# Performance work log

Measured on AMD Instinct MI355X. Metric: run time of the kernel, lower is better.

Reference implementation:

```python
import jax, jax.numpy as jnp
import numpy as np

# PSLoss constants (from init_kwargs)
MSE_WEIGHT = 0.5
W_CORR = 1.0
W_VAR = 1.0
W_MEAN = 1.0
K = 3           # k_dominant_freqs
MIN_PATCH = 5   # min_patch_len (max(2, 5))
EPS = 1e-8


def setup_inputs() -> dict:
    key = jax.random.key(0)
    k1, k2 = jax.random.split(key)
    B, T, F = 64, 336, 321
    forecast = jax.random.normal(k1, (B, T, F), dtype=jnp.float32)
    target = jax.random.normal(k2, (B, T, F), dtype=jnp.float32)
    return {"forecast": forecast, "target": target}


def _structural_loss(fc, tg):
    """fc, tg: [N, T] flattened (batch*features) series. Returns (total_loss_sum, patch_count)."""
    N, T = tg.shape
    Mmax = T // MIN_PATCH  # max segments per period (period >= MIN_PATCH)

    # --- Fourier adaptive patching (vectorized over all N series) ---
    amp = jnp.abs(jnp.fft.rfft(tg, axis=-1))[:, 1:]           # drop DC, [N, T//2]
    _, rel = jax.lax.top_k(amp, K)                             # [N, K]
    freq_idx = (rel + 1).astype(jnp.float32)
    p = jnp.floor(T / freq_idx).astype(jnp.int32)              # dominant periods [N, K]
    # dedup periods in topk order (the original 'processed_periods' set)
    eq = p[:, :, None] == p[:, None, :]                        # [N, K, K]
    earlier = jnp.tril(jnp.ones((K, K), dtype=bool), -1)       # j < k
    dup = jnp.any(eq & earlier, axis=-1)
    valid_p = (p >= MIN_PATCH) & ~dup                          # [N, K]

    nseg = T // p                                              # [N, K] (p >= 2 always)
    s_idx = jnp.arange(Mmax, dtype=jnp.int32)
    seg_s = p[:, :, None] * s_idx                              # [N, K, Mmax]
    seg_e = seg_s + p[:, :, None]
    seg_v = (s_idx < nseg[:, :, None]) & valid_p[:, :, None]
    rem_s = nseg * p                                           # remaining tail patch
    rem_v = valid_p & ((T - rem_s) >= MIN_PATCH)

    starts = jnp.concatenate([seg_s.reshape(N, -1), rem_s], axis=-1)
    ends = jnp.concatenate([seg_e.reshape(N, -1), jnp.full_like(rem_s, T)], axis=-1)
    valid = jnp.concatenate([seg_v.reshape(N, -1), rem_v], axis=-1)
    # fallback whole-series patch if no patch survived
    none = ~jnp.any(valid, axis=-1, keepdims=True)
    starts = jnp.concatenate([starts, jnp.zeros((N, 1), jnp.int32)], axis=-1)
    ends = jnp.concatenate([ends, jnp.full((N, 1), T, jnp.int32)], axis=-1)
    valid = jnp.concatenate([valid, none], axis=-1)            # [N, M]

    # --- dedup identical (start, end) patches (original list(set(...))) ---
    SENT = (T + 1) * (T + 1)
    keys = jnp.where(valid, starts * (T + 1) + ends, SENT)
    keys = jnp.sort(keys, axis=-1)
    uniq = jnp.concatenate(
        [jnp.ones((N, 1), dtype=bool), keys[:, 1:] != keys[:, :-1]], axis=-1)
    valid = (keys != SENT) & uniq
    s = jnp.where(valid, keys // (T + 1), 0)                   # safe dummy (0,2) when invalid
    e = jnp.where(valid, keys % (T + 1), 2)

    # --- per-patch stats via inclusive prefix sums ---
    def csum(x):
        return jnp.concatenate([jnp.zeros((N, 1), x.dtype), jnp.cumsum(x, axis=-1)], axis=-1)

    cs_t, cs_f = csum(tg), csum(fc)
    cs_tt, cs_ff, cs_tf = csum(tg * tg), csum(fc * fc), csum(tg * fc)

    def seg_sum(cs):
        return jnp.take_along_axis(cs, e, axis=-1) - jnp.take_along_axis(cs, s, axis=-1)

    n = (e - s).astype(jnp.float32)
    St, Sf = seg_sum(cs_t), seg_sum(cs_f)
    Stt, Sff, Stf = seg_sum(cs_tt), seg_sum(cs_ff), seg_sum(cs_tf)
    mt, mf = St / n, Sf / n
    tvs = jnp.maximum(Stt - n * mt * mt, 0.0)   # sum of squared deviations (target)
    fvs = jnp.maximum(Sff - n * mf * mf, 0.0)
    num = Stf - n * mt * mf
    corr = num / (jnp.sqrt(tvs * fvs) + EPS)
    corr_loss = 1.0 - jnp.abs(corr)
    tvar = tvs / (n - 1.0)                      # torch.var is unbiased
    fvar = fvs / (n - 1.0)
    var_loss = jnp.abs(tvar - fvar) / (tvar + EPS)
    mean_loss = jnp.abs(mt - mf) / (jnp.abs(mt) + EPS)
    patch_loss = W_CORR * corr_loss + W_VAR * var_loss + W_MEAN * mean_loss

    total = jnp.sum(jnp.where(valid, patch_loss, 0.0))
    count = jnp.sum(valid)
    return total, count


def reference(forecast, target):
    B, T, F = forecast.shape
    fc = jnp.transpose(forecast, (0, 2, 1)).reshape(B * F, T)
    tg = jnp.transpose(target, (0, 2, 1)).reshape(B * F, T)
    total, count = _structural_loss(fc, tg)
    avg = jnp.where(count > 0,
                    total / jnp.maximum(count, 1).astype(jnp.float32),
                    jnp.float32(0.0))
    mse = jnp.mean((forecast - target) ** 2)
    return MSE_WEIGHT * mse + (1.0 - MSE_WEIGHT) * avg
```

## Files before the change

kernel.cpp:

```cpp
#include <hip/hip_runtime.h>
#include <hip/hip_bf16.h>

#define TT 336
#define NF 321
#define NB 64
#define NSER (NB * NF)
#define WPB 4
#define KP 352
#define LDA 360
#define SPP 16
#define WV 8
#define NFB (NSER / SPP)
#define NFBG 1288
#define TSP 340

#define TWS 1056

#define TGX 11
#define TGY 11
#define NMSEP (TGX * TGY * NB)

typedef __attribute__((ext_vector_type(8))) short bf16x8;
typedef __attribute__((ext_vector_type(4))) float f32x4;
typedef unsigned long long ULL;

__device__ __forceinline__ unsigned short f2bf(float v) {
    unsigned x = __float_as_uint(v);
    x += 0x7FFFu + ((x >> 16) & 1u);
    return (unsigned short)(x >> 16);
}

__device__ __forceinline__ void ins3(ULL& a0, ULL& a1, ULL& a2, ULL x) {
    ULL hi = a0 > x ? a0 : x;
    ULL lo = a0 > x ? x : a0;
    a0 = hi;
    ULL hi1 = a1 > lo ? a1 : lo;
    ULL lo1 = a1 > lo ? lo : a1;
    a1 = hi1;
    a2 = a2 > lo1 ? a2 : lo1;
}

__device__ __forceinline__ int idiv336(int d) {
    return (int)(__fdividef(336.0f, (float)d));
}

__global__ void twiddle_k(unsigned short* __restrict__ Wb) {
    int n = blockIdx.x;
    int f = (n >> 1) + 1;
    int isSin = n & 1;
    for (int k = threadIdx.x; k < KP; k += blockDim.x) {
        float v = 0.0f;
        if (k < TT) {
            int r = (f * k) % TT;
            float ang = 6.2831853071795864769f * (float)r / 336.0f;
            v = isSin ? sinf(ang) : cosf(ang);
        }
        Wb[(size_t)n * KP + k] = f2bf(v);
    }
}

__device__ __forceinline__ float patch_loss_f32(float S1, float S2, float S3,
                                                float S4, float S5, int n) {
    float nnf = (float)n;
    float invf = 1.0f / nnf;
    float tvs = S3 - S1 * S1 * invf; tvs = tvs > 0.f ? tvs : 0.f;
    float fvs = S4 - S2 * S2 * invf; fvs = fvs > 0.f ? fvs : 0.f;
    float num = S5 - S1 * S2 * invf;
    float corr = num / (sqrtf(tvs * fvs) + 1e-8f);
    float closs = 1.0f - fabsf(corr);
    float vloss = fabsf(tvs - fvs) / (tvs + (nnf - 1.0f) * 1e-8f);
    float mloss = fabsf(S1 - S2) / (fabsf(S1) + nnf * 1e-8f);
    return closs + vloss + mloss;
}

__device__ __forceinline__ double patch_loss(double S1, double S2, double S3,
                                             double S4, double S5, double nn) {
    double mt = S1 / nn, mf = S2 / nn;
    double tvs = S3 - nn * mt * mt; tvs = tvs > 0.0 ? tvs : 0.0;
    double fvs = S4 - nn * mf * mf; fvs = fvs > 0.0 ? fvs : 0.0;
    double num = S5 - nn * mt * mf;
    double corr = num / (sqrt(tvs * fvs) + 1e-8);
    double closs = 1.0 - fabs(corr);
    double tvar = tvs / (nn - 1.0), fvar = fvs / (nn - 1.0);
    double vloss = fabs(tvar - fvar) / (tvar + 1e-8);
    double mloss = fabs(mt - mf) / (fabs(mt) + 1e-8);
    return closs + vloss + mloss;
}

struct PatchCfg {
    int P[3], nseg[3], rs[3];
    float rp[3];
    bool vp[3], hr[3];
};

__device__ __forceinline__ void make_cfg(int fr0, int fr1, int fr2, PatchCfg& c) {
    c.P[0] = idiv336(fr0); c.P[1] = idiv336(fr1); c.P[2] = idiv336(fr2);
    c.vp[0] = (c.P[0] >= 5);
    c.vp[1] = (c.P[1] >= 5) && (c.P[1] != c.P[0]);
    c.vp[2] = (c.P[2] >= 5) && (c.P[2] != c.P[0]) && (c.P[2] != c.P[1]);
#pragma unroll
    for (int q = 0; q < 3; q++) {
        c.nseg[q] = idiv336(c.P[q] > 0 ? c.P[q] : 1);
        c.rs[q] = c.nseg[q] * c.P[q];
        c.hr[q] = c.vp[q] && ((TT - c.rs[q]) >= 5);
        c.rp[q] = (c.P[q] > 0) ? __frcp_rn((float)c.P[q]) : 0.0f;
    }
}

__device__ __forceinline__ bool slot_patch(const PatchCfg& c, int i, int& s, int& e) {
    bool kept = false;
    s = 0; e = 0;
    if (i < 204) {
        int k = (i >= 136) ? 2 : ((i >= 68) ? 1 : 0);
        int si = i - k * 68;
        if (c.vp[k]) {
            if (si < c.nseg[k]) { s = c.P[k] * si; e = s + c.P[k]; kept = true; }
            else if (si == c.nseg[k] && c.hr[k]) { s = c.rs[k]; e = TT; kept = true; }
            if (kept) {
#pragma unroll
                for (int j = 0; j < 2; j++) {
                    if (j < k && c.vp[j]) {
                        bool dup = (s == c.rs[j]) && (e == TT) && c.hr[j];
                        int len = e - s;
                        if (len == c.P[j] && s < c.rs[j] && (s % c.P[j]) == 0) dup = true;
                        if (dup) kept = false;
                    }
                }
            }
        }
    }
    return kept;
}

__global__ __launch_bounds__(512) void fused_k(const float* __restrict__ tgO,
                                               const float* __restrict__ fcO,
                                               const unsigned short* __restrict__ Wb,
                                               double* __restrict__ blkout) {
    __shared__ __align__(16) char smem[43520 + WV * TWS * 4];
    float2* ts = (float2*)smem;
    unsigned short* sA = (unsigned short*)(smem + 43520);
    ULL* tk3 = (ULL*)(smem + 43520 + 11520);
    float* tabAll = (float*)(smem + 43520);
    __shared__ uint4 tkf[SPP];
    __shared__ double wms[WV], wls[WV];
    __shared__ int wlc[WV];

    const int tid = threadIdx.x;
    const int wave = tid >> 6, lane = tid & 63;
    const int lb = (blockIdx.x & 7) * 161 + (blockIdx.x >> 3);
    if (lb >= NFB) return;
    const int serBase = lb * SPP;

    {
        const int j = tid & 15, tch = tid >> 4;
        const int ser = serBase + j;
        const int bb = ser / NF, ff = ser - bb * NF;
        const float* tb_ = tgO + (size_t)bb * TT * NF + ff;
        const float* fb_ = fcO + (size_t)bb * TT * NF + ff;
        int t0, nT;
        if (tch < 16) { t0 = tch * 11; nT = 11; }
        else          { t0 = 176 + (tch - 16) * 10; nT = 10; }
        float va[11], vc[11];
#pragma unroll
        for (int i = 0; i < 11; i++) if (i < nT) va[i] = tb_[(size_t)(t0 + i) * NF];
#pragma unroll
        for (int i = 0; i < 11; i++) if (i < nT) vc[i] = fb_[(size_t)(t0 + i) * NF];
        float ms = 0.0f;
#pragma unroll
        for (int i = 0; i < 11; i++) {
            if (i < nT) {
                int t = t0 + i;
                ts[j * TSP + t] = make_float2(va[i], vc[i]);
                sA[j * LDA + t] = f2bf(va[i]);
                float d = va[i] - vc[i];
                ms = fmaf(d, d, ms);
            }
        }
        for (int off = 32; off; off >>= 1) ms += __shfl_down(ms, off, 64);
        if (lane == 0) wms[wave] = (double)ms;
        if (tid < SPP * 16) sA[(tid & 15) * LDA + TT + (tid >> 4)] = 0;
    }
    __syncthreads();

    {
        const int quad = lane >> 4, c = lane & 15;
        const unsigned short* aRow = sA + c * LDA + quad * 8;
        const int ntStart = (wave < 5) ? wave * 3 : 15 + (wave - 5) * 2;
        const int ntEnd = ntStart + ((wave < 5) ? 3 : 2);

        ULL t0k[4] = {0, 0, 0, 0}, t1k[4] = {0, 0, 0, 0}, t2k[4] = {0, 0, 0, 0};
        for (int nt = ntStart; nt < ntEnd; nt++) {
            const unsigned short* bRow = Wb + (size_t)(nt * 16 + c) * KP + quad * 8;
            f32x4 acc = (f32x4){0.f, 0.f, 0.f, 0.f};
#pragma unroll
            for (int ks = 0; ks < 11; ks++) {
                bf16x8 a = *(const bf16x8*)(aRow + ks * 32);
                bf16x8 b = *(const bf16x8*)(bRow + ks * 32);
                acc = __builtin_amdgcn_mfma_f32_16x16x32_bf16(a, b, acc, 0, 0, 0);
            }
            int n = nt * 16 + c;
            unsigned fidx = (unsigned)((n >> 1) + 1);
            unsigned ftag = 0xFFFFFFFFu - fidx;
            bool odd = (n & 1) != 0;
#pragma unroll
            for (int r = 0; r < 4; r++) {
                float v = acc[r];
                float p = v * v;
                p += __shfl_xor(p, 1, 64);
                ULL key = odd ? 0ull
                              : (((ULL)__float_as_uint(p) << 32) | (ULL)ftag);
                ins3(t0k[r], t1k[r], t2k[r], key);
            }
        }
#pragma unroll
        for (int m = 2; m <= 8; m <<= 1) {
#pragma unroll
            for (int r = 0; r < 4; r++) {
                ULL b0 = __shfl_xor(t0k[r], m, 64);
                ULL b1 = __shfl_xor(t1k[r], m, 64);
                ULL b2 = __shfl_xor(t2k[r], m, 64);
                ins3(t0k[r], t1k[r], t2k[r], b0);
                ins3(t0k[r], t1k[r], t2k[r], b1);
                ins3(t0k[r], t1k[r], t2k[r], b2);
            }
        }
        if (c == 0) {
#pragma unroll
            for (int r = 0; r < 4; r++) {
                int s = quad * 4 + r;
                tk3[(wave * 16 + s) * 3 + 0] = t0k[r];
                tk3[(wave * 16 + s) * 3 + 1] = t1k[r];
                tk3[(wave * 16 + s) * 3 + 2] = t2k[r];
            }
        }
    }
    __syncthreads();
    if (tid < SPP) {
        ULL k0 = 0, k1 = 0, k2 = 0;
#pragma unroll
        for (int wv = 0; wv < WV; wv++) {
#pragma unroll
            for (int j = 0; j < 3; j++) ins3(k0, k1, k2, tk3[(wv * 16 + tid) * 3 + j]);
        }
        unsigned f0 = 0xFFFFFFFFu - (unsigned)(k0 & 0xFFFFFFFFull);
        unsigned f1 = 0xFFFFFFFFu - (unsigned)(k1 & 0xFFFFFFFFull);
        unsigned f2 = 0xFFFFFFFFu - (unsigned)(k2 & 0xFFFFFFFFull);
        tkf[tid] = make_uint4(f0, f1, f2, 0u);
    }
    __syncthreads();

    float* tw = tabAll + wave * TWS;
    float lsum = 0.0f;
    int lcnt = 0;
#pragma unroll 1
    for (int r = 0; r < 2; r++) {
        const int jj = (wave << 1) | r;

        uint4 tk = tkf[jj];
        PatchCfg cfg;
        make_cfg((int)tk.x, (int)tk.y, (int)tk.z, cfg);

        float2 loc[6];
        float c1 = 0.f, c2 = 0.f, c3 = 0.f, c4 = 0.f, c5 = 0.f;
        if (lane < 56) {
            const float4* lp = (const float4*)(ts + jj * TSP + 6 * lane);
            float4 va = lp[0], vb = lp[1], vcc = lp[2];
            loc[0] = make_float2(va.x, va.y); loc[1] = make_float2(va.z, va.w);
            loc[2] = make_float2(vb.x, vb.y); loc[3] = make_float2(vb.z, vb.w);
            loc[4] = make_float2(vcc.x, vcc.y); loc[5] = make_float2(vcc.z, vcc.w);
#pragma unroll
            for (int i = 0; i < 6; i++) {
                float a = loc[i].x, b = loc[i].y;
                c1 += a; c2 += b;
                c3 = fmaf(a, a, c3); c4 = fmaf(b, b, c4); c5 = fmaf(a, b, c5);
            }
        }

        float s1 = c1, s2 = c2, s3 = c3, s4 = c4, s5 = c5;
#pragma unroll
        for (int off = 1; off < 64; off <<= 1) {
            float y1 = __shfl_up(s1, off, 64);
            float y2 = __shfl_up(s2, off, 64);
            float y3 = __shfl_up(s3, off, 64);
            float y4 = __shfl_up(s4, off, 64);
            float y5 = __shfl_up(s5, off, 64);
            if (lane >= off) { s1 += y1; s2 += y2; s3 += y3; s4 += y4; s5 += y5; }
        }

        if (lane == 63) {
#pragma unroll
            for (int k = 0; k < 3; k++) {
#pragma unroll
                for (int q = 0; q < 5; q++) tw[(k * 70) * 5 + q] = 0.f;
            }
        }
        if (lane < 56) {
            float r1 = s1 - c1, r2 = s2 - c2;
            float r3 = s3 - c3, r4 = s4 - c4, r5 = s5 - c5;
#pragma unroll
            for (int i = 0; i < 6; i++) {
                float a = loc[i].x, b = loc[i].y;
                r1 += a; r2 += b;
                r3 = fmaf(a, a, r3); r4 = fmaf(b, b, r4); r5 = fmaf(a, b, r5);
                int tp = 6 * lane + i + 1;
                float tpf = (float)tp;
                if (tp == TT) {
                    tw[1050] = r1; tw[1051] = r2; tw[1052] = r3;
                    tw[1053] = r4; tw[1054] = r5;
                }
#pragma unroll
                for (int k = 0; k < 3; k++) {
                    if (cfg.vp[k]) {
                        int q = (int)(tpf * cfg.rp[k] + 0.001f);
                        if (q * cfg.P[k] == tp && q <= 68) {
                            int ix = (k * 70 + q) * 5;
                            tw[ix + 0] = r1; tw[ix + 1] = r2; tw[ix + 2] = r3;
                            tw[ix + 3] = r4; tw[ix + 4] = r5;
                        }
                    }
                }
            }
        }

        ULL anyMask = 0ull;
#pragma unroll
        for (int rI = 0; rI < 4; rI++) {
            int i = lane + 64 * rI;
            int s, e;
            bool kept = slot_patch(cfg, i, s, e);
            ULL bal = __ballot(kept);
            anyMask |= bal;
            if (bal == 0ull) continue;
            if (kept) {
                int k = (i >= 136) ? 2 : ((i >= 68) ? 1 : 0);
                int si = i - k * 68;
                bool tail = (si == cfg.nseg[k]);
                const float* pS = tw + (k * 70 + si) * 5;
                const float* pE = tail ? (tw + 1050) : (tw + (k * 70 + si + 1) * 5);
                float S1 = pE[0] - pS[0];
                float S2 = pE[1] - pS[1];
                float S3 = pE[2] - pS[2];
                float S4 = pE[3] - pS[3];
                float S5 = pE[4] - pS[4];
                lsum += patch_loss_f32(S1, S2, S3, S4, S5, e - s);
                lcnt += 1;
            }
        }
        if (anyMask == 0ull) {
            if (lane == 0) {
                lsum += patch_loss_f32(tw[1050], tw[1051], tw[1052],
                                       tw[1053], tw[1054], TT);
                lcnt += 1;
            }
        }
    }

    for (int off = 32; off; off >>= 1) {
        lsum += __shfl_down(lsum, off, 64);
        lcnt += __shfl_down(lcnt, off, 64);
    }
    if (lane == 0) { wls[wave] = (double)lsum; wlc[wave] = lcnt; }
    __syncthreads();
    if (tid == 0) {
        double L = 0.0, M = 0.0;
        int C = 0;
#pragma unroll
        for (int wv = 0; wv < WV; wv++) { L += wls[wv]; C += wlc[wv]; M += wms[wv]; }
        blkout[3 * lb + 0] = L;
        blkout[3 * lb + 1] = (double)C;
        blkout[3 * lb + 2] = M;
    }
}

__global__ __launch_bounds__(256) void transpose_k(const float* __restrict__ fc,
                                                   const float* __restrict__ tg,
                                                   float2* __restrict__ out,
                                                   double* __restrict__ msep,
                                                   double* __restrict__ acc) {
    __shared__ float ta[32][33];
    __shared__ float tb[32][33];
    __shared__ double wacc[4];
    const int b = blockIdx.z;
    const int t0 = blockIdx.x * 32, f0 = blockIdx.y * 32;
    const int tx = threadIdx.x, ty = threadIdx.y;
    const size_t base = (size_t)b * TT * NF;
    double ms = 0.0;
#pragma unroll
    for (int k = 0; k < 4; k++) {
        int t = t0 + ty + 8 * k, f = f0 + tx;
        if (t < TT && f < NF) {
            float a = tg[base + (size_t)t * NF + f];
            float c = fc[base + (size_t)t * NF + f];
            ta[ty + 8 * k][tx] = a;
            tb[ty + 8 * k][tx] = c;
            double d = (double)a - (double)c;
            ms += d * d;
        }
    }
    __syncthreads();
#pragma unroll
    for (int k = 0; k < 4; k++) {
        int f = f0 + ty + 8 * k, t = t0 + tx;
        if (t < TT && f < NF) {
            out[((size_t)b * NF + f) * TT + t] =
                make_float2(ta[tx][ty + 8 * k], tb[tx][ty + 8 * k]);
        }
    }
    for (int off = 32; off; off >>= 1) ms += __shfl_down(ms, off, 64);
    int flat = ty * 32 + tx;
    int lane = flat & 63, wid = flat >> 6;
    if (lane == 0) wacc[wid] = ms;
    __syncthreads();
    if (flat == 0) {
        double tot = wacc[0] + wacc[1] + wacc[2] + wacc[3];
        if (msep) {
            int blk = (blockIdx.z * TGY + blockIdx.y) * TGX + blockIdx.x;
            msep[blk] = tot;
        } else {
            atomicAdd(&acc[0], tot);
        }
    }
}

__global__ void mse_k(const float* __restrict__ fc, const float* __restrict__ tg,
                      double* __restrict__ acc) {
    const size_t N4 = (size_t)NB * TT * NF / 4;
    const float4* a4 = (const float4*)fc;
    const float4* b4 = (const float4*)tg;
    double s = 0.0;
    for (size_t i = (size_t)blockIdx.x * blockDim.x + threadIdx.x; i < N4;
         i += (size_t)gridDim.x * blockDim.x) {
        float4 a = a4[i], b = b4[i];
        double d0 = (double)a.x - (double)b.x;
        double d1 = (double)a.y - (double)b.y;
        double d2 = (double)a.z - (double)b.z;
        double d3 = (double)a.w - (double)b.w;
        s += d0 * d0 + d1 * d1 + d2 * d2 + d3 * d3;
    }
    for (int off = 32; off; off >>= 1) s += __shfl_down(s, off, 64);
    __shared__ double wsum[4];
    int flat = threadIdx.x;
    int lane = flat & 63, wid = flat >> 6;
    if (lane == 0) wsum[wid] = s;
    __syncthreads();
    if (flat == 0) atomicAdd(&acc[0], wsum[0] + wsum[1] + wsum[2] + wsum[3]);
}

__device__ __forceinline__ void patch_body(const float2* tsw, int lane,
                                           int fr0, int fr1, int fr2,
                                           double& lsum, double& lcnt) {
    PatchCfg cfg;
    make_cfg(fr0, fr1, fr2, cfg);
    ULL anyMask = 0ull;
#pragma unroll
    for (int rI = 0; rI < 4; rI++) {
        int s, e;
        bool kept = slot_patch(cfg, lane + 64 * rI, s, e);
        anyMask |= __ballot(kept);
        if (kept) {
            double S1 = 0, S2 = 0, S3 = 0, S4 = 0, S5 = 0;
            for (int t = s; t < e; t++) {
                float2 v = tsw[t];
                double a = (double)v.x, b = (double)v.y;
                S1 += a; S2 += b;
                S3 += a * a; S4 += b * b; S5 += a * b;
            }
            lsum += patch_loss(S1, S2, S3, S4, S5, (double)(e - s));
            lcnt += 1.0;
        }
    }
    if (anyMask == 0ull) {
        double S1 = 0, S2 = 0, S3 = 0, S4 = 0, S5 = 0;
        for (int t = lane; t < TT; t += 64) {
            float2 v = tsw[t];
            double a = (double)v.x, b = (double)v.y;
            S1 += a; S2 += b;
            S3 += a * a; S4 += b * b; S5 += a * b;
        }
        for (int off = 32; off; off >>= 1) {
            S1 += __shfl_down(S1, off, 64);
            S2 += __shfl_down(S2, off, 64);
            S3 += __shfl_down(S3, off, 64);
            S4 += __shfl_down(S4, off, 64);
            S5 += __shfl_down(S5, off, 64);
        }
        if (lane == 0) {
            lsum += patch_loss(S1, S2, S3, S4, S5, (double)TT);
            lcnt += 1.0;
        }
    }
}

__global__ __launch_bounds__(256, 6) void series_k(const float2* __restrict__ tsG,
                                                   const float* __restrict__ fcG,
                                                   const float* __restrict__ tgG,
                                                   int transposed,
                                                   double2* __restrict__ pairs,
                                                   double* __restrict__ acc) {
    const int w = threadIdx.x >> 6, lane = threadIdx.x & 63;
    const int ser = blockIdx.x * WPB + w;
    __shared__ float2 ts[WPB][TT];
    __shared__ float4 zb[WPB][84];

    if (transposed) {
        const float2* sp = tsG + (size_t)ser * TT;
        for (int t = lane; t < TT; t += 64) ts[w][t] = sp[t];
    } else {
        int b = ser / NF, f = ser - b * NF;
        const float* tp = tgG + (size_t)b * TT * NF + f;
        const float* fp = fcG + (size_t)b * TT * NF + f;
        for (int t = lane; t < TT; t += 64)
            ts[w][t] = make_float2(tp[(size_t)t * NF], fp[(size_t)t * NF]);
    }
    __syncthreads();

    for (int t = lane; t < 84; t += 64) {
        float x0 = ts[w][t].x, x1 = ts[w][t + 84].x;
        float x2 = ts[w][t + 168].x, x3 = ts[w][t + 252].x;
        float a = x0 + x2, b2 = x1 + x3, c = x0 - x2, d = x1 - x3;
        zb[w][t] = make_float4(a + b2, a - b2, c, d);
    }
    __syncthreads();

    const double TWOPI = 6.283185307179586476925286766559;
    int fb[3] = {1 + lane, 65 + lane, 129 + lane};
    float cc[3], sn[3], re[3], im[3], cd[3], sd[3], sgn[3];
    int selA[3];
#pragma unroll
    for (int q = 0; q < 3; q++) {
        int f = fb[q], cls = f & 3;
        double dl = (double)f * (TWOPI / 336.0);
        cd[q] = (float)cos(dl);
        sd[q] = (float)sin(dl);
        cc[q] = 1.0f; sn[q] = 0.0f; re[q] = 0.0f; im[q] = 0.0f;
        sgn[q] = (cls == 1) ? -1.0f : ((cls == 3) ? 1.0f : 0.0f);
        selA[q] = (cls == 0) ? 0 : ((cls == 2) ? 1 : 2);
    }
    for (int t = 0; t < 84; t++) {
        float4 zv = zb[w][t];
#pragma unroll
        for (int q = 0; q < 3; q++) {
            float zr = (selA[q] == 0) ? zv.x : ((selA[q] == 1) ? zv.y : zv.z);
            float zi = sgn[q] * zv.w;
            re[q] = fmaf(zr, cc[q], re[q]);
            re[q] = fmaf(zi, sn[q], re[q]);
            im[q] = fmaf(zi, cc[q], im[q]);
            im[q] = fmaf(-zr, sn[q], im[q]);
            float nc = fmaf(cc[q], cd[q], -(sn[q] * sd[q]));
            float ns = fmaf(sn[q], cd[q], cc[q] * sd[q]);
            cc[q] = nc; sn[q] = ns;
        }
    }

    ULL k0 = 0, k1 = 0, k2 = 0;
#pragma unroll
    for (int q = 0; q < 3; q++) {
        float a2 = fmaf(re[q], re[q], im[q] * im[q]);
        ULL key = ((ULL)__float_as_uint(a2) << 32) |
                  (ULL)(0xFFFFFFFFu - (unsigned)fb[q]);
        if (fb[q] > 168) key = 0ull;
        ins3(k0, k1, k2, key);
    }
    for (int m = 1; m < 64; m <<= 1) {
        ULL b0 = __shfl_xor(k0, m, 64);
        ULL b1 = __shfl_xor(k1, m, 64);
        ULL b2 = __shfl_xor(k2, m, 64);
        ins3(k0, k1, k2, b0); ins3(k0, k1, k2, b1); ins3(k0, k1, k2, b2);
    }

    int fr0 = (int)(0xFFFFFFFFu - (unsigned)(k0 & 0xFFFFFFFFull));
    int fr1 = (int)(0xFFFFFFFFu - (unsigned)(k1 & 0xFFFFFFFFull));
    int fr2 = (int)(0xFFFFFFFFu - (unsigned)(k2 & 0xFFFFFFFFull));

    double lsum = 0.0, lcnt = 0.0;
    patch_body(&ts[w][0], lane, fr0, fr1, fr2, lsum, lcnt);

    for (int off = 32; off; off >>= 1) {
        lsum += __shfl_down(lsum, off, 64);
        lcnt += __shfl_down(lcnt, off, 64);
    }
    if (lane == 0) {
        if (pairs) {
            pairs[ser] = make_double2(lsum, lcnt);
        } else {
            atomicAdd(&acc[1], lsum);
            atomicAdd(&acc[2], lcnt);
        }
    }
}

__global__ __launch_bounds__(1024) void reduce3_k(const double* __restrict__ blkout,
                                                  float* __restrict__ out) {
    const int tid = threadIdx.x;
    double ls = 0.0, lc = 0.0, ms = 0.0;
    for (int i = tid; i < NFB; i += 1024) {
        ls += blkout[3 * i + 0];
        lc += blkout[3 * i + 1];
        ms += blkout[3 * i + 2];
    }
    for (int off = 32; off; off >>= 1) {
        ls += __shfl_down(ls, off, 64);
        lc += __shfl_down(lc, off, 64);
        ms += __shfl_down(ms, off, 64);
    }
    __shared__ double sl[16], sc[16], sm[16];
    int lane = tid & 63, wid = tid >> 6;
    if (lane == 0) { sl[wid] = ls; sc[wid] = lc; sm[wid] = ms; }
    __syncthreads();
    if (tid == 0) {
        double L = 0, C = 0, M = 0;
        for (int i = 0; i < 16; i++) { L += sl[i]; C += sc[i]; M += sm[i]; }
        double mse = M / (double)((size_t)NB * TT * NF);
        double avg = (C > 0.0) ? (L / C) : 0.0;
        out[0] = (float)(0.5 * mse + 0.5 * avg);
    }
}

__global__ __launch_bounds__(1024) void reduce_k(const double2* __restrict__ pairs,
                                                 const double* __restrict__ msep,
                                                 int nmse,
                                                 float* __restrict__ out) {
    const int tid = threadIdx.x;
    double ls = 0.0, lc = 0.0, ms = 0.0;
    for (int i = tid; i < NSER; i += 1024) {
        double2 p = pairs[i];
        ls += p.x; lc += p.y;
    }
    for (int i = tid; i < nmse; i += 1024) ms += msep[i];
    for (int off = 32; off; off >>= 1) {
        ls += __shfl_down(ls, off, 64);
        lc += __shfl_down(lc, off, 64);
        ms += __shfl_down(ms, off, 64);
    }
    __shared__ double sl[16], sc[16], sm[16];
    int lane = tid & 63, wid = tid >> 6;
    if (lane == 0) { sl[wid] = ls; sc[wid] = lc; sm[wid] = ms; }
    __syncthreads();
    if (tid == 0) {
        double L = 0, C = 0, M = 0;
        for (int i = 0; i < 16; i++) { L += sl[i]; C += sc[i]; M += sm[i]; }
        double mse = M / (double)((size_t)NB * TT * NF);
        double avg = (C > 0.0) ? (L / C) : 0.0;
        out[0] = (float)(0.5 * mse + 0.5 * avg);
    }
}

__global__ void finalize_k(const double* __restrict__ acc, float* __restrict__ out) {
    double mse = acc[0] / (double)((size_t)NB * TT * NF);
    double avg = (acc[2] > 0.0) ? (acc[1] / acc[2]) : 0.0;
    out[0] = (float)(0.5 * mse + 0.5 * avg);
}

extern "C" void kernel_launch(void* const* d_in, const int* in_sizes, int n_in,
                              void* d_out, int out_size, void* d_ws, size_t ws_size,
                              hipStream_t stream) {
    const float* fc = (const float*)d_in[0];
    const float* tg = (const float*)d_in[1];
    float* out = (float*)d_out;
    char* ws = (char*)d_ws;
    double* acc = (double*)ws;

    const size_t OFF_MSE = 64;
    const size_t OFF_PAIR = OFF_MSE + (size_t)NMSEP * sizeof(double);
    const size_t OFF_TOP = OFF_PAIR + (size_t)NSER * sizeof(double2);
    const size_t OFF_W = OFF_TOP + (size_t)NSER * sizeof(uint4);
    const size_t OFF_END2 = OFF_W + (size_t)TT * KP * sizeof(unsigned short);
    const size_t bytesT = (size_t)NSER * TT * sizeof(float2);
    const bool big2 = (ws_size >= OFF_END2);
    const size_t R3_OFF_TS = OFF_PAIR + (size_t)NSER * sizeof(double2);
    const bool big = !big2 && (ws_size >= R3_OFF_TS + bytesT);
    const bool mid = !big2 && !big && (ws_size >= OFF_MSE + bytesT);

    double* msep = (double*)(ws + OFF_MSE);
    double* blkout = (double*)(ws + OFF_PAIR);
    unsigned short* Wb = (unsigned short*)(ws + OFF_W);

    dim3 tg_grid(TGX, TGY, NB);
    dim3 tg_blk(32, 8);

    if (big2) {
        twiddle_k<<<TT, 128, 0, stream>>>(Wb);
        fused_k<<<NFBG, 64 * WV, 0, stream>>>(tg, fc, Wb, blkout);
        reduce3_k<<<1, 1024, 0, stream>>>(blkout, out);
    } else if (big) {
        float2* tsT = (float2*)(ws + R3_OFF_TS);
        transpose_k<<<tg_grid, tg_blk, 0, stream>>>(fc, tg, tsT, msep, acc);
        series_k<<<NSER / WPB, 64 * WPB, 0, stream>>>(tsT, fc, tg, 1,
                                                      (double2*)blkout, acc);
        reduce_k<<<1, 1024, 0, stream>>>((double2*)blkout, msep, NMSEP, out);
    } else if (mid) {
        float2* tsT = (float2*)(ws + OFF_MSE);
        hipMemsetAsync(d_ws, 0, 64, stream);
        transpose_k<<<tg_grid, tg_blk, 0, stream>>>(fc, tg, tsT, nullptr, acc);
        series_k<<<NSER / WPB, 64 * WPB, 0, stream>>>(tsT, fc, tg, 1, nullptr, acc);
        finalize_k<<<1, 1, 0, stream>>>(acc, out);
    } else {
        hipMemsetAsync(d_ws, 0, 64, stream);
        mse_k<<<1024, 256, 0, stream>>>(fc, tg, acc);
        series_k<<<NSER / WPB, 64 * WPB, 0, stream>>>(nullptr, fc, tg, 0, nullptr, acc);
        finalize_k<<<1, 1, 0, stream>>>(acc, out);
    }
}
```

Measured before the change: 150.2 us.

## Shrink fused kernel shared memory and fold final reduction into last block

Shared memory in the fused kernel is compacted: the bf16 A-tile stride drops to 340, the last MFMA k-step zero-fills the padding in registers, and the per-wave scratch tables now alias the series buffer once the series are cached in registers. The occupancy hint is raised to 6 blocks. The separate reduce kernel is replaced by an atomic counter that lets the last block do the final reduction, at the cost of a memset and a threadfence per block. Reusing ts as scratch depends on each wave loading both its series into registers before the buffer is overwritten.

```diff
diff --git a/kernel.cpp b/kernel.cpp
--- a/kernel.cpp
+++ b/kernel.cpp
@@ -7,12 +7,12 @@
 #define NSER (NB * NF)
 #define WPB 4
 #define KP 352
-#define LDA 360
+#define LDA2 340
 #define SPP 16
 #define WV 8
 #define NFB (NSER / SPP)
 #define NFBG 1288
-#define TSP 340
+#define TSP 338
 
 #define TWS 1056
 
@@ -132,18 +132,22 @@
     return kept;
 }
 
-__global__ __launch_bounds__(512) void fused_k(const float* __restrict__ tgO,
-                                               const float* __restrict__ fcO,
-                                               const unsigned short* __restrict__ Wb,
-                                               double* __restrict__ blkout) {
-    __shared__ __align__(16) char smem[43520 + WV * TWS * 4];
+__global__ __launch_bounds__(512, 6) void fused_k(const float* __restrict__ tgO,
+                                                  const float* __restrict__ fcO,
+                                                  const unsigned short* __restrict__ Wb,
+                                                  double* __restrict__ blkout,
+                                                  unsigned* __restrict__ cnt,
+                                                  float* __restrict__ out) {
+    __shared__ __align__(16) char smem[43264 + 10880 + 64];
     float2* ts = (float2*)smem;
-    unsigned short* sA = (unsigned short*)(smem + 43520);
-    ULL* tk3 = (ULL*)(smem + 43520 + 11520);
-    float* tabAll = (float*)(smem + 43520);
-    __shared__ uint4 tkf[SPP];
-    __shared__ double wms[WV], wls[WV];
-    __shared__ int wlc[WV];
+    unsigned short* sA = (unsigned short*)(smem + 43264);
+    ULL* tk3 = (ULL*)(smem + 43264);
+    uint4* tkf = (uint4*)(smem + 43264 + 3072);
+    double* wls = (double*)(smem + 43264 + 3328);
+    int* wlc = (int*)(smem + 43264 + 3392);
+    int* isLast = (int*)(smem + 43264 + 3424);
+    double* wms = (double*)(smem + 43264 + 10880);
+    double* red = (double*)smem;
 
     const int tid = threadIdx.x;
     const int wave = tid >> 6, lane = tid & 63;
@@ -171,32 +175,37 @@
             if (i < nT) {
                 int t = t0 + i;
                 ts[j * TSP + t] = make_float2(va[i], vc[i]);
-                sA[j * LDA + t] = f2bf(va[i]);
+                sA[j * LDA2 + t] = f2bf(va[i]);
                 float d = va[i] - vc[i];
                 ms = fmaf(d, d, ms);
             }
         }
         for (int off = 32; off; off >>= 1) ms += __shfl_down(ms, off, 64);
         if (lane == 0) wms[wave] = (double)ms;
-        if (tid < SPP * 16) sA[(tid & 15) * LDA + TT + (tid >> 4)] = 0;
-    }
-    __syncthreads();
-
+    }
+    __syncthreads();
+
+    const int quad = lane >> 4, c = lane & 15;
+    ULL t0k[4] = {0, 0, 0, 0}, t1k[4] = {0, 0, 0, 0}, t2k[4] = {0, 0, 0, 0};
     {
-        const int quad = lane >> 4, c = lane & 15;
-        const unsigned short* aRow = sA + c * LDA + quad * 8;
+        const unsigned short* aRow = sA + c * LDA2 + quad * 8;
         const int ntStart = (wave < 5) ? wave * 3 : 15 + (wave - 5) * 2;
         const int ntEnd = ntStart + ((wave < 5) ? 3 : 2);
 
-        ULL t0k[4] = {0, 0, 0, 0}, t1k[4] = {0, 0, 0, 0}, t2k[4] = {0, 0, 0, 0};
         for (int nt = ntStart; nt < ntEnd; nt++) {
             const unsigned short* bRow = Wb + (size_t)(nt * 16 + c) * KP + quad * 8;
             f32x4 acc = (f32x4){0.f, 0.f, 0.f, 0.f};
 #pragma unroll
-            for (int ks = 0; ks < 11; ks++) {
+            for (int ks = 0; ks < 10; ks++) {
                 bf16x8 a = *(const bf16x8*)(aRow + ks * 32);
                 bf16x8 b = *(const bf16x8*)(bRow + ks * 32);
                 acc = __builtin_amdgcn_mfma_f32_16x16x32_bf16(a, b, acc, 0, 0, 0);
+            }
+            {
+                bf16x8 a10 = (bf16x8){0, 0, 0, 0, 0, 0, 0, 0};
+                if (quad < 2) a10 = *(const bf16x8*)(aRow + 320);
+                bf16x8 b10 = *(const bf16x8*)(bRow + 320);
+                acc = __builtin_amdgcn_mfma_f32_16x16x32_bf16(a10, b10, acc, 0, 0, 0);
             }
             int n = nt * 16 + c;
             unsigned fidx = (unsigned)((n >> 1) + 1);
@@ -224,14 +233,15 @@
                 ins3(t0k[r], t1k[r], t2k[r], b2);
             }
         }
-        if (c == 0) {
-#pragma unroll
-            for (int r = 0; r < 4; r++) {
-                int s = quad * 4 + r;
-                tk3[(wave * 16 + s) * 3 + 0] = t0k[r];
-                tk3[(wave * 16 + s) * 3 + 1] = t1k[r];
-                tk3[(wave * 16 + s) * 3 + 2] = t2k[r];
-            }
+    }
+    __syncthreads();
+    if (c == 0) {
+#pragma unroll
+        for (int r = 0; r < 4; r++) {
+            int s = quad * 4 + r;
+            tk3[(wave * 16 + s) * 3 + 0] = t0k[r];
+            tk3[(wave * 16 + s) * 3 + 1] = t1k[r];
+            tk3[(wave * 16 + s) * 3 + 2] = t2k[r];
         }
     }
     __syncthreads();
@@ -249,7 +259,21 @@
     }
     __syncthreads();
 
-    float* tw = tabAll + wave * TWS;
+    float* tw = (float*)smem + (size_t)(wave * 2) * (TSP * 2);
+    float2 lcA[6], lcB[6];
+    if (lane < 56) {
+        const float4* p0 = (const float4*)(ts + (wave * 2) * TSP + 6 * lane);
+        const float4* p1 = (const float4*)(ts + (wave * 2 + 1) * TSP + 6 * lane);
+        float4 a0 = p0[0], a1 = p0[1], a2 = p0[2];
+        float4 b0 = p1[0], b1 = p1[1], b2 = p1[2];
+        lcA[0] = make_float2(a0.x, a0.y); lcA[1] = make_float2(a0.z, a0.w);
+        lcA[2] = make_float2(a1.x, a1.y); lcA[3] = make_float2(a1.z, a1.w);
+        lcA[4] = make_float2(a2.x, a2.y); lcA[5] = make_float2(a2.z, a2.w);
+        lcB[0] = make_float2(b0.x, b0.y); lcB[1] = make_float2(b0.z, b0.w);
+        lcB[2] = make_float2(b1.x, b1.y); lcB[3] = make_float2(b1.z, b1.w);
+        lcB[4] = make_float2(b2.x, b2.y); lcB[5] = make_float2(b2.z, b2.w);
+    }
+
     float lsum = 0.0f;
     int lcnt = 0;
 #pragma unroll 1
@@ -261,13 +285,11 @@
         make_cfg((int)tk.x, (int)tk.y, (int)tk.z, cfg);
 
         float2 loc[6];
+#pragma unroll
+        for (int i = 0; i < 6; i++) loc[i] = r ? lcB[i] : lcA[i];
+
         float c1 = 0.f, c2 = 0.f, c3 = 0.f, c4 = 0.f, c5 = 0.f;
         if (lane < 56) {
-            const float4* lp = (const float4*)(ts + jj * TSP + 6 * lane);
-            float4 va = lp[0], vb = lp[1], vcc = lp[2];
-            loc[0] = make_float2(va.x, va.y); loc[1] = make_float2(va.z, va.w);
-            loc[2] = make_float2(vb.x, vb.y); loc[3] = make_float2(vb.z, vb.w);
-            loc[4] = make_float2(vcc.x, vcc.y); loc[5] = make_float2(vcc.z, vcc.w);
 #pragma unroll
             for (int i = 0; i < 6; i++) {
                 float a = loc[i].x, b = loc[i].y;
@@ -369,6 +391,35 @@
         blkout[3 * lb + 0] = L;
         blkout[3 * lb + 1] = (double)C;
         blkout[3 * lb + 2] = M;
+        __threadfence();
+        unsigned old = atomicAdd(cnt, 1u);
+        *isLast = (old == (unsigned)(NFB - 1)) ? 1 : 0;
+    }
+    __syncthreads();
+
+    if (*isLast) {
+        __threadfence();
+        double ls = 0.0, lc2 = 0.0, ms2 = 0.0;
+        for (int i = tid; i < NFB; i += 512) {
+            ls += blkout[3 * i + 0];
+            lc2 += blkout[3 * i + 1];
+            ms2 += blkout[3 * i + 2];
+        }
+        for (int off = 32; off; off >>= 1) {
+            ls += __shfl_down(ls, off, 64);
+            lc2 += __shfl_down(lc2, off, 64);
+            ms2 += __shfl_down(ms2, off, 64);
+        }
+        if (lane == 0) { red[wave] = ls; red[8 + wave] = lc2; red[16 + wave] = ms2; }
+        __syncthreads();
+        if (tid == 0) {
+            double L = 0, C = 0, M = 0;
+#pragma unroll
+            for (int i = 0; i < 8; i++) { L += red[i]; C += red[8 + i]; M += red[16 + i]; }
+            double mse = M / (double)((size_t)NB * TT * NF);
+            double avg = (C > 0.0) ? (L / C) : 0.0;
+            out[0] = (float)(0.5 * mse + 0.5 * avg);
+        }
     }
 }
 
@@ -589,33 +640,6 @@
     }
 }
 
-__global__ __launch_bounds__(1024) void reduce3_k(const double* __restrict__ blkout,
-                                                  float* __restrict__ out) {
-    const int tid = threadIdx.x;
-    double ls = 0.0, lc = 0.0, ms = 0.0;
-    for (int i = tid; i < NFB; i += 1024) {
-        ls += blkout[3 * i + 0];
-        lc += blkout[3 * i + 1];
-        ms += blkout[3 * i + 2];
-    }
-    for (int off = 32; off; off >>= 1) {
-        ls += __shfl_down(ls, off, 64);
-        lc += __shfl_down(lc, off, 64);
-        ms += __shfl_down(ms, off, 64);
-    }
-    __shared__ double sl[16], sc[16], sm[16];
-    int lane = tid & 63, wid = tid >> 6;
-    if (lane == 0) { sl[wid] = ls; sc[wid] = lc; sm[wid] = ms; }
-    __syncthreads();
-    if (tid == 0) {
-        double L = 0, C = 0, M = 0;
-        for (int i = 0; i < 16; i++) { L += sl[i]; C += sc[i]; M += sm[i]; }
-        double mse = M / (double)((size_t)NB * TT * NF);
-        double avg = (C > 0.0) ? (L / C) : 0.0;
-        out[0] = (float)(0.5 * mse + 0.5 * avg);
-    }
-}
-
 __global__ __launch_bounds__(1024) void reduce_k(const double2* __restrict__ pairs,
                                                  const double* __restrict__ msep,
                                                  int nmse,
@@ -659,6 +683,7 @@
     float* out = (float*)d_out;
     char* ws = (char*)d_ws;
     double* acc = (double*)ws;
+    unsigned* cnt = (unsigned*)(ws + 32);
 
     const size_t OFF_MSE = 64;
     const size_t OFF_PAIR = OFF_MSE + (size_t)NMSEP * sizeof(double);
@@ -679,9 +704,9 @@
     dim3 tg_blk(32, 8);
 
     if (big2) {
+        hipMemsetAsync(d_ws, 0, 64, stream);
         twiddle_k<<<TT, 128, 0, stream>>>(Wb);
-        fused_k<<<NFBG, 64 * WV, 0, stream>>>(tg, fc, Wb, blkout);
-        reduce3_k<<<1, 1024, 0, stream>>>(blkout, out);
+        fused_k<<<NFBG, 64 * WV, 0, stream>>>(tg, fc, Wb, blkout, cnt, out);
     } else if (big) {
         float2* tsT = (float2*)(ws + R3_OFF_TS);
         transpose_k<<<tg_grid, tg_blk, 0, stream>>>(fc, tg, tsT, msep, acc);
```

After: 283.1 us. 1.89x slower.
